# Kernel optimization log

Hardware: AMD Instinct MI355X
Metric: run time of the kernel (lower is better)

The kernel has to match this reference:

```python
import jax, jax.numpy as jnp
import numpy as np

N, E = 50000, 800000
ND, ED, HD = 128, 32, 256  # node_dim, edge_dim, hidden_dim

def silu(v):
    return v * jax.nn.sigmoid(v)

def setup_inputs() -> dict:
    key = jax.random.key(0)
    ks = jax.random.split(key, 16)
    s = lambda fan_in: 1.0 / np.sqrt(fan_in)
    inp = {
        'h': jax.random.normal(ks[0], (N, ND), jnp.float32),
        'x': jax.random.normal(ks[1], (N, 3), jnp.float32),
        'edge_index': jax.random.randint(ks[2], (2, E), 0, N, jnp.int64),
        'edge_attr': jax.random.normal(ks[3], (E, ED), jnp.float32),
        # msg_mlp: Linear(2*ND+1+ED, HD) -> SiLU -> Linear(HD, HD) -> SiLU
        'mW1': jax.random.normal(ks[4], (2 * ND + 1 + ED, HD), jnp.float32) * s(2 * ND + 1 + ED),
        'mb1': jnp.zeros((HD,), jnp.float32),
        'mW2': jax.random.normal(ks[5], (HD, HD), jnp.float32) * s(HD),
        'mb2': jnp.zeros((HD,), jnp.float32),
        # node_mlp: Linear(ND+HD, HD) -> SiLU -> Linear(HD, ND)
        'nW1': jax.random.normal(ks[6], (ND + HD, HD), jnp.float32) * s(ND + HD),
        'nb1': jnp.zeros((HD,), jnp.float32),
        'nW2': jax.random.normal(ks[7], (HD, ND), jnp.float32) * s(HD),
        'nb2': jnp.zeros((ND,), jnp.float32),
        # coord_mlp: Linear(HD, HD) -> SiLU -> Linear(HD, 1, bias=False)
        'cW1': jax.random.normal(ks[8], (HD, HD), jnp.float32) * s(HD),
        'cb1': jnp.zeros((HD,), jnp.float32),
        'cW2': jax.random.normal(ks[9], (HD, 1), jnp.float32) * s(HD),
        # LayerNorm(ND)
        'gamma': jnp.ones((ND,), jnp.float32),
        'beta': jnp.zeros((ND,), jnp.float32),
    }
    return inp

def reference(h, x, edge_index, edge_attr,
              mW1, mb1, mW2, mb2,
              nW1, nb1, nW2, nb2,
              cW1, cb1, cW2, gamma, beta):
    row, col = edge_index[0], edge_index[1]
    n = h.shape[0]
    dx = x[row] - x[col]                                   # [E,3]
    dist_sq = jnp.sum(dx * dx, axis=-1, keepdims=True) + 1e-8
    edge_in = jnp.concatenate([h[row], h[col], dist_sq, edge_attr], axis=-1)
    m = silu(edge_in @ mW1 + mb1)
    m = silu(m @ mW2 + mb2)                                # m_ij: [E,HD]
    m_i = jax.ops.segment_sum(m, row, num_segments=n)      # [N,HD]
    coef = silu(m @ cW1 + cb1) @ cW2                       # [E,1]
    x_agg = jax.ops.segment_sum(dx * coef, row, num_segments=n)
    x_out = x + x_agg
    h_in = jnp.concatenate([h, m_i], axis=-1)
    h_res = h + (silu(h_in @ nW1 + nb1) @ nW2 + nb2)
    mu = jnp.mean(h_res, axis=-1, keepdims=True)
    var = jnp.mean((h_res - mu) ** 2, axis=-1, keepdims=True)
    h_out = (h_res - mu) / jnp.sqrt(var + 1e-5) * gamma + beta
    return h_out, x_out
```

## Files before the change

kernel.cpp:

```cpp
#include <hip/hip_runtime.h>

#define ND 128
#define ED 32
#define HD 256
#define ASTR 296
#define NSTR 392

typedef short bf16x8 __attribute__((ext_vector_type(8)));
typedef float f32x4 __attribute__((ext_vector_type(4)));

__device__ __forceinline__ float silu_f(float v) {
  return v / (1.0f + __expf(-v));
}

__device__ __forceinline__ unsigned short bf_hi(float f) {
  unsigned int u = __float_as_uint(f);
  return (unsigned short)((u + 0x7FFFu + ((u >> 16) & 1u)) >> 16);
}
__device__ __forceinline__ float bf_to_f(unsigned short s) {
  return __uint_as_float(((unsigned int)s) << 16);
}
__device__ __forceinline__ void split2(float f, unsigned short& hi, unsigned short& lo) {
  hi = bf_hi(f);
  lo = bf_hi(f - bf_to_f(hi));
}
__device__ __forceinline__ void store_split4(unsigned short* hp, unsigned short* lp, float4 v) {
  ushort4 h4, l4;
  split2(v.x, h4.x, l4.x); split2(v.y, h4.y, l4.y);
  split2(v.z, h4.z, l4.z); split2(v.w, h4.w, l4.w);
  *reinterpret_cast<ushort4*>(hp) = h4;
  *reinterpret_cast<ushort4*>(lp) = l4;
}

__global__ void prep_frag(const float* __restrict__ W, unsigned short* __restrict__ Fh,
                          unsigned short* __restrict__ Fl, int Keff, int Ncols, int S,
                          int skiprow)
{
  int idx = blockIdx.x * 256 + threadIdx.x;
  int NT = Ncols >> 4;
  int total = S * NT * 64;
  if (idx >= total) return;
  int lane = idx & 63;
  int k0 = (idx / (NT * 64)) * 32 + ((lane >> 4) << 3);
  int n = ((idx >> 6) % NT) * 16 + (lane & 15);
  size_t base = (size_t)idx * 8;
  for (int j = 0; j < 8; ++j) {
    int k = k0 + j;
    float v = 0.f;
    if (k < Keff) {
      int wk = (skiprow >= 0 && k >= skiprow) ? (k + 1) : k;
      v = W[(size_t)wk * Ncols + n];
    }
    unsigned short hi, lo; split2(v, hi, lo);
    Fh[base + j] = hi; Fl[base + j] = lo;
  }
}

template<int STRIDE, int NT, int NTW>
__device__ __forceinline__ void mfma_gemm(const unsigned short* __restrict__ Ahi,
                                          const unsigned short* __restrict__ Alo,
                                          const unsigned short* __restrict__ Bh,
                                          const unsigned short* __restrict__ Bl,
                                          int S, int wave, int lane, f32x4 acc[4][NTW])
{
  const int tx = lane & 15, tz = lane >> 4;
  for (int s = 0; s < S; ++s) {
    bf16x8 bh[NTW], bl[NTW], ah[4], al[4];
    #pragma unroll
    for (int nt = 0; nt < NTW; ++nt) {
      size_t bidx = ((size_t)(s * NT + wave * NTW + nt) * 64 + lane) * 8;
      bh[nt] = *reinterpret_cast<const bf16x8*>(Bh + bidx);
      bl[nt] = *reinterpret_cast<const bf16x8*>(Bl + bidx);
    }
    const int koff = s * 32 + tz * 8;
    #pragma unroll
    for (int mt = 0; mt < 4; ++mt) {
      size_t aoff = (size_t)(mt * 16 + tx) * STRIDE + koff;
      ah[mt] = *reinterpret_cast<const bf16x8*>(Ahi + aoff);
      al[mt] = *reinterpret_cast<const bf16x8*>(Alo + aoff);
    }
    #pragma unroll
    for (int mt = 0; mt < 4; ++mt) {
      #pragma unroll
      for (int nt = 0; nt < NTW; ++nt) {
        acc[mt][nt] = __builtin_amdgcn_mfma_f32_16x16x32_bf16(ah[mt], bh[nt], acc[mt][nt], 0, 0, 0);
        acc[mt][nt] = __builtin_amdgcn_mfma_f32_16x16x32_bf16(ah[mt], bl[nt], acc[mt][nt], 0, 0, 0);
        acc[mt][nt] = __builtin_amdgcn_mfma_f32_16x16x32_bf16(al[mt], bh[nt], acc[mt][nt], 0, 0, 0);
      }
    }
  }
}

__global__ __launch_bounds__(512, 4)
void egnn_edge_mfma(const float* __restrict__ h, const float* __restrict__ x,
                    const int* __restrict__ eidx, const float* __restrict__ eattr,
                    const float* __restrict__ mW1, const float* __restrict__ mb1,
                    const float* __restrict__ mb2, const float* __restrict__ cb1,
                    const float* __restrict__ cW2,
                    const unsigned short* __restrict__ W1h, const unsigned short* __restrict__ W1l,
                    const unsigned short* __restrict__ W2h, const unsigned short* __restrict__ W2l,
                    const unsigned short* __restrict__ C1h, const unsigned short* __restrict__ C1l,
                    float* __restrict__ m_i, float* __restrict__ x_agg, int E)
{
  __shared__ unsigned short Ahi[64][ASTR];
  __shared__ unsigned short Alo[64][ASTR];
  __shared__ int   sRow[64];
  __shared__ float sDx0[64], sDx1[64], sDx2[64], sDist[64], sCoef[64];

  const int t  = threadIdx.x;
  const int e0 = blockIdx.x * 64;
  if (t < 64) sCoef[t] = 0.f;

  {
    const int e = t >> 3, part = t & 7;
    const int ge = e0 + e;
    if (ge < E) {
      const int r = eidx[ge], c = eidx[E + ge];
      const float* hsrc = (part < 4) ? (h + (size_t)r * ND + (part & 3) * 32)
                                     : (h + (size_t)c * ND + (part & 3) * 32);
      const int cb = (part < 4 ? 0 : 128) + (part & 3) * 32;
      #pragma unroll
      for (int i = 0; i < 8; ++i) {
        float4 v = reinterpret_cast<const float4*>(hsrc)[i];
        store_split4(&Ahi[e][cb + i * 4], &Alo[e][cb + i * 4], v);
      }
      float4 av = reinterpret_cast<const float4*>(eattr + (size_t)ge * ED)[part];
      store_split4(&Ahi[e][256 + part * 4], &Alo[e][256 + part * 4], av);
      if (part == 0) {
        sRow[e] = r;
        float d0 = x[3*(size_t)r+0] - x[3*(size_t)c+0];
        float d1 = x[3*(size_t)r+1] - x[3*(size_t)c+1];
        float d2 = x[3*(size_t)r+2] - x[3*(size_t)c+2];
        sDx0[e] = d0; sDx1[e] = d1; sDx2[e] = d2;
        sDist[e] = d0*d0 + d1*d1 + d2*d2 + 1e-8f;
      }
    }
  }
  __syncthreads();

  const int lane = t & 63, wave = t >> 6;
  const int tx = lane & 15, tz = lane >> 4;
  const int c0 = wave * 32 + tx;
  const int c1 = c0 + 16;

  f32x4 acc[4][2];

  {
    const float b0v = mb1[c0], b1v = mb1[c1];
    const float wA = mW1[(size_t)256 * HD + c0];
    const float wB = mW1[(size_t)256 * HD + c1];
    #pragma unroll
    for (int mt = 0; mt < 4; ++mt)
      #pragma unroll
      for (int r = 0; r < 4; ++r) {
        const float d = sDist[mt * 16 + tz * 4 + r];
        acc[mt][0][r] = b0v + d * wA;
        acc[mt][1][r] = b1v + d * wB;
      }
  }
  mfma_gemm<ASTR, 16, 2>(&Ahi[0][0], &Alo[0][0], W1h, W1l, 9, wave, lane, acc);
  __syncthreads();
  #pragma unroll
  for (int mt = 0; mt < 4; ++mt)
    #pragma unroll
    for (int r = 0; r < 4; ++r) {
      const int row = mt * 16 + tz * 4 + r;
      unsigned short hi, lo;
      split2(silu_f(acc[mt][0][r]), hi, lo);
      Ahi[row][c0] = hi; Alo[row][c0] = lo;
      split2(silu_f(acc[mt][1][r]), hi, lo);
      Ahi[row][c1] = hi; Alo[row][c1] = lo;
    }
  __syncthreads();

  {
    const float b0v = mb2[c0], b1v = mb2[c1];
    #pragma unroll
    for (int mt = 0; mt < 4; ++mt)
      #pragma unroll
      for (int r = 0; r < 4; ++r) { acc[mt][0][r] = b0v; acc[mt][1][r] = b1v; }
  }
  mfma_gemm<ASTR, 16, 2>(&Ahi[0][0], &Alo[0][0], W2h, W2l, 8, wave, lane, acc);
  #pragma unroll
  for (int mt = 0; mt < 4; ++mt)
    #pragma unroll
    for (int r = 0; r < 4; ++r) {
      acc[mt][0][r] = silu_f(acc[mt][0][r]);
      acc[mt][1][r] = silu_f(acc[mt][1][r]);
      const int row = mt * 16 + tz * 4 + r;
      if (e0 + row < E) {
        const size_t rn = (size_t)sRow[row] * HD;
        unsafeAtomicAdd(&m_i[rn + c0], acc[mt][0][r]);
        unsafeAtomicAdd(&m_i[rn + c1], acc[mt][1][r]);
      }
    }
  __syncthreads();
  #pragma unroll
  for (int mt = 0; mt < 4; ++mt)
    #pragma unroll
    for (int r = 0; r < 4; ++r) {
      const int row = mt * 16 + tz * 4 + r;
      unsigned short hi, lo;
      split2(acc[mt][0][r], hi, lo);
      Ahi[row][c0] = hi; Alo[row][c0] = lo;
      split2(acc[mt][1][r], hi, lo);
      Ahi[row][c1] = hi; Alo[row][c1] = lo;
    }
  __syncthreads();

  {
    const float b0v = cb1[c0], b1v = cb1[c1];
    #pragma unroll
    for (int mt = 0; mt < 4; ++mt)
      #pragma unroll
      for (int r = 0; r < 4; ++r) { acc[mt][0][r] = b0v; acc[mt][1][r] = b1v; }
  }
  mfma_gemm<ASTR, 16, 2>(&Ahi[0][0], &Alo[0][0], C1h, C1l, 8, wave, lane, acc);
  {
    const float w20 = cW2[c0], w21 = cW2[c1];
    #pragma unroll
    for (int mt = 0; mt < 4; ++mt)
      #pragma unroll
      for (int r = 0; r < 4; ++r) {
        float v = silu_f(acc[mt][0][r]) * w20 + silu_f(acc[mt][1][r]) * w21;
        v += __shfl_xor(v, 1); v += __shfl_xor(v, 2);
        v += __shfl_xor(v, 4); v += __shfl_xor(v, 8);
        if (tx == 0) atomicAdd(&sCoef[mt * 16 + tz * 4 + r], v);
      }
  }
  __syncthreads();
  if (t < 64 && e0 + t < E) {
    const float cf = sCoef[t];
    const size_t rn = 3 * (size_t)sRow[t];
    unsafeAtomicAdd(&x_agg[rn + 0], sDx0[t] * cf);
    unsafeAtomicAdd(&x_agg[rn + 1], sDx1[t] * cf);
    unsafeAtomicAdd(&x_agg[rn + 2], sDx2[t] * cf);
  }
}

__global__ __launch_bounds__(512, 2)
void egnn_node_mfma(const float* __restrict__ h, const float* __restrict__ m_i,
                    const unsigned short* __restrict__ N1h, const unsigned short* __restrict__ N1l,
                    const unsigned short* __restrict__ N2h, const unsigned short* __restrict__ N2l,
                    const float* __restrict__ nb1, const float* __restrict__ nb2,
                    const float* __restrict__ gamma, const float* __restrict__ beta,
                    float* __restrict__ hout, int N)
{
  __shared__ unsigned short Ahi[64][NSTR];
  __shared__ unsigned short Alo[64][NSTR];
  __shared__ float sSum[64], sSum2[64];

  const int t  = threadIdx.x;
  const int n0 = blockIdx.x * 64;
  if (t < 64) { sSum[t] = 0.f; sSum2[t] = 0.f; }

  {
    const int e = t >> 3, part = t & 7;
    const int n = n0 + e;
    if (n < N) {
      #pragma unroll
      for (int i = 0; i < 4; ++i) {
        float4 v = reinterpret_cast<const float4*>(h + (size_t)n * ND + part * 16)[i];
        store_split4(&Ahi[e][part * 16 + i * 4], &Alo[e][part * 16 + i * 4], v);
      }
      #pragma unroll
      for (int i = 0; i < 8; ++i) {
        float4 v = reinterpret_cast<const float4*>(m_i + (size_t)n * HD + part * 32)[i];
        store_split4(&Ahi[e][128 + part * 32 + i * 4], &Alo[e][128 + part * 32 + i * 4], v);
      }
    }
  }
  __syncthreads();

  const int lane = t & 63, wave = t >> 6;
  const int tx = lane & 15, tz = lane >> 4;

  {
    const int c0 = wave * 32 + tx, c1 = c0 + 16;
    f32x4 acc[4][2];
    const float b0v = nb1[c0], b1v = nb1[c1];
    #pragma unroll
    for (int mt = 0; mt < 4; ++mt)
      #pragma unroll
      for (int r = 0; r < 4; ++r) { acc[mt][0][r] = b0v; acc[mt][1][r] = b1v; }
    mfma_gemm<NSTR, 16, 2>(&Ahi[0][0], &Alo[0][0], N1h, N1l, 12, wave, lane, acc);
    __syncthreads();
    #pragma unroll
    for (int mt = 0; mt < 4; ++mt)
      #pragma unroll
      for (int r = 0; r < 4; ++r) {
        const int row = mt * 16 + tz * 4 + r;
        unsigned short hi, lo;
        split2(silu_f(acc[mt][0][r]), hi, lo);
        Ahi[row][c0] = hi; Alo[row][c0] = lo;
        split2(silu_f(acc[mt][1][r]), hi, lo);
        Ahi[row][c1] = hi; Alo[row][c1] = lo;
      }
    __syncthreads();
  }

  const int col = wave * 16 + tx;
  f32x4 a2[4][1];
  {
    const float bv = nb2[col];
    #pragma unroll
    for (int mt = 0; mt < 4; ++mt)
      #pragma unroll
      for (int r = 0; r < 4; ++r) a2[mt][0][r] = bv;
  }
  mfma_gemm<NSTR, 8, 1>(&Ahi[0][0], &Alo[0][0], N2h, N2l, 8, wave, lane, a2);

  const float g  = gamma[col];
  const float bt = beta[col];
  float vv[4][4];
  #pragma unroll
  for (int mt = 0; mt < 4; ++mt)
    #pragma unroll
    for (int r = 0; r < 4; ++r) {
      const int row = mt * 16 + tz * 4 + r;
      const int n = n0 + row;
      const float hv = (n < N) ? h[(size_t)n * ND + col] : 0.f;
      const float v = a2[mt][0][r] + hv;
      vv[mt][r] = v;
      float s1 = v, s2 = v * v;
      s1 += __shfl_xor(s1, 1); s1 += __shfl_xor(s1, 2);
      s1 += __shfl_xor(s1, 4); s1 += __shfl_xor(s1, 8);
      s2 += __shfl_xor(s2, 1); s2 += __shfl_xor(s2, 2);
      s2 += __shfl_xor(s2, 4); s2 += __shfl_xor(s2, 8);
      if (tx == 0) {
        atomicAdd(&sSum[row],  s1);
        atomicAdd(&sSum2[row], s2);
      }
    }
  __syncthreads();
  #pragma unroll
  for (int mt = 0; mt < 4; ++mt)
    #pragma unroll
    for (int r = 0; r < 4; ++r) {
      const int row = mt * 16 + tz * 4 + r;
      const int n = n0 + row;
      if (n < N) {
        const float mu   = sSum[row] * (1.f / 128.f);
        const float var  = sSum2[row] * (1.f / 128.f) - mu * mu;
        const float rstd = rsqrtf(var + 1e-5f);
        hout[(size_t)n * ND + col] = (vv[mt][r] - mu) * rstd * g + bt;
      }
    }
}

__global__ void egnn_xout_kernel(const float* __restrict__ x, const float* __restrict__ x_agg,
                                 float* __restrict__ xout, int total)
{
  int i = blockIdx.x * 256 + threadIdx.x;
  if (i < total) xout[i] = x[i] + x_agg[i];
}

extern "C" void kernel_launch(void* const* d_in, const int* in_sizes, int n_in,
                              void* d_out, int out_size, void* d_ws, size_t ws_size,
                              hipStream_t stream)
{
  const float* h     = (const float*)d_in[0];
  const float* x     = (const float*)d_in[1];
  const int*   eidx  = (const int*)  d_in[2];
  const float* eattr = (const float*)d_in[3];
  const float* mW1   = (const float*)d_in[4];
  const float* mb1   = (const float*)d_in[5];
  const float* mW2   = (const float*)d_in[6];
  const float* mb2   = (const float*)d_in[7];
  const float* nW1   = (const float*)d_in[8];
  const float* nb1   = (const float*)d_in[9];
  const float* nW2   = (const float*)d_in[10];
  const float* nb2   = (const float*)d_in[11];
  const float* cW1   = (const float*)d_in[12];
  const float* cb1   = (const float*)d_in[13];
  const float* cW2   = (const float*)d_in[14];
  const float* gamma = (const float*)d_in[15];
  const float* beta  = (const float*)d_in[16];

  const int N = in_sizes[0] / ND;
  const int E = in_sizes[2] / 2;

  float* m_i   = (float*)d_ws;
  float* x_agg = m_i + (size_t)N * HD;
  unsigned short* fr = (unsigned short*)(x_agg + (size_t)N * 3);

  const int SZ_W1 = 9  * 16 * 64 * 8;
  const int SZ_W2 = 8  * 16 * 64 * 8;
  const int SZ_N1 = 12 * 16 * 64 * 8;
  const int SZ_N2 = 8  * 8  * 64 * 8;
  unsigned short* W1h = fr; fr += SZ_W1;
  unsigned short* W1l = fr; fr += SZ_W1;
  unsigned short* W2h = fr; fr += SZ_W2;
  unsigned short* W2l = fr; fr += SZ_W2;
  unsigned short* C1h = fr; fr += SZ_W2;
  unsigned short* C1l = fr; fr += SZ_W2;
  unsigned short* N1h = fr; fr += SZ_N1;
  unsigned short* N1l = fr; fr += SZ_N1;
  unsigned short* N2h = fr; fr += SZ_N2;
  unsigned short* N2l = fr; fr += SZ_N2;

  float* hout = (float*)d_out;
  float* xout = hout + (size_t)N * ND;

  hipMemsetAsync(m_i,   0, (size_t)N * HD * sizeof(float), stream);
  hipMemsetAsync(x_agg, 0, (size_t)N * 3  * sizeof(float), stream);

  prep_frag<<<(9*16*64  + 255)/256, 256, 0, stream>>>(mW1, W1h, W1l, 288, 256,  9, 256);
  prep_frag<<<(8*16*64  + 255)/256, 256, 0, stream>>>(mW2, W2h, W2l, 256, 256,  8,  -1);
  prep_frag<<<(8*16*64  + 255)/256, 256, 0, stream>>>(cW1, C1h, C1l, 256, 256,  8,  -1);
  prep_frag<<<(12*16*64 + 255)/256, 256, 0, stream>>>(nW1, N1h, N1l, 384, 256, 12,  -1);
  prep_frag<<<(8*8*64   + 255)/256, 256, 0, stream>>>(nW2, N2h, N2l, 256, 128,  8,  -1);

  egnn_edge_mfma<<<(E + 63) / 64, 512, 0, stream>>>(
      h, x, eidx, eattr, mW1, mb1, mb2, cb1, cW2,
      W1h, W1l, W2h, W2l, C1h, C1l, m_i, x_agg, E);
  egnn_node_mfma<<<(N + 63) / 64, 512, 0, stream>>>(
      h, m_i, N1h, N1l, N2h, N2l, nb1, nb2, gamma, beta, hout, N);
  egnn_xout_kernel<<<(N * 3 + 255) / 256, 256, 0, stream>>>(x, x_agg, xout, N * 3);
}
```

Baseline: 1.415 ms.

## Presplit node features to bf16 hi/lo, use hardware bf16 convert, unroll GEMM

Adds a presplit kernel that converts h into bf16 hi/lo arrays once, so the edge and node kernels copy pre-split halves instead of re-splitting the gathered features per edge. Replaces the software round-to-nearest bf16 split with the v_cvt_pk_bf16_f32 instruction. Makes the GEMM k-step count a template parameter with full unrolling and raises wave priority around the MFMA block with s_setprio. It also moves the m_i atomics after the LDS write of the second-layer output. The trade-offs are an extra kernel and workspace buffer, more registers and code from the unroll, and possible rounding-mode differences in the conversion.

```diff
diff --git a/kernel.cpp b/kernel.cpp
--- a/kernel.cpp
+++ b/kernel.cpp
@@ -13,23 +13,38 @@
   return v / (1.0f + __expf(-v));
 }
 
-__device__ __forceinline__ unsigned short bf_hi(float f) {
-  unsigned int u = __float_as_uint(f);
-  return (unsigned short)((u + 0x7FFFu + ((u >> 16) & 1u)) >> 16);
-}
-__device__ __forceinline__ float bf_to_f(unsigned short s) {
-  return __uint_as_float(((unsigned int)s) << 16);
-}
-__device__ __forceinline__ void split2(float f, unsigned short& hi, unsigned short& lo) {
-  hi = bf_hi(f);
-  lo = bf_hi(f - bf_to_f(hi));
+__device__ __forceinline__ unsigned int cvt_pk_bf16(float a, float b) {
+  unsigned int r;
+  asm("v_cvt_pk_bf16_f32 %0, %1, %2" : "=v"(r) : "v"(a), "v"(b));
+  return r;
+}
+__device__ __forceinline__ void split_pk(float f0, float f1, unsigned int& hw, unsigned int& lw) {
+  hw = cvt_pk_bf16(f0, f1);
+  float h0 = __uint_as_float(hw << 16);
+  float h1 = __uint_as_float(hw & 0xFFFF0000u);
+  lw = cvt_pk_bf16(f0 - h0, f1 - h1);
+}
+__device__ __forceinline__ void split1(float v, unsigned short& hs, unsigned short& ls) {
+  unsigned int hw = cvt_pk_bf16(v, v);
+  float hf = __uint_as_float(hw << 16);
+  unsigned int lw = cvt_pk_bf16(v - hf, v - hf);
+  hs = (unsigned short)hw; ls = (unsigned short)lw;
 }
 __device__ __forceinline__ void store_split4(unsigned short* hp, unsigned short* lp, float4 v) {
-  ushort4 h4, l4;
-  split2(v.x, h4.x, l4.x); split2(v.y, h4.y, l4.y);
-  split2(v.z, h4.z, l4.z); split2(v.w, h4.w, l4.w);
-  *reinterpret_cast<ushort4*>(hp) = h4;
-  *reinterpret_cast<ushort4*>(lp) = l4;
+  unsigned int hw0, lw0, hw1, lw1;
+  split_pk(v.x, v.y, hw0, lw0);
+  split_pk(v.z, v.w, hw1, lw1);
+  *reinterpret_cast<uint2*>(hp) = make_uint2(hw0, hw1);
+  *reinterpret_cast<uint2*>(lp) = make_uint2(lw0, lw1);
+}
+
+__global__ void presplit_kernel(const float* __restrict__ src, unsigned short* __restrict__ dh,
+                                unsigned short* __restrict__ dl, int total4)
+{
+  int i = blockIdx.x * 256 + threadIdx.x;
+  if (i >= total4) return;
+  float4 v = reinterpret_cast<const float4*>(src)[i];
+  store_split4(dh + (size_t)i * 4, dl + (size_t)i * 4, v);
 }
 
 __global__ void prep_frag(const float* __restrict__ W, unsigned short* __restrict__ Fh,
@@ -51,19 +66,20 @@
       int wk = (skiprow >= 0 && k >= skiprow) ? (k + 1) : k;
       v = W[(size_t)wk * Ncols + n];
     }
-    unsigned short hi, lo; split2(v, hi, lo);
+    unsigned short hi, lo; split1(v, hi, lo);
     Fh[base + j] = hi; Fl[base + j] = lo;
   }
 }
 
-template<int STRIDE, int NT, int NTW>
-__device__ __forceinline__ void mfma_gemm(const unsigned short* __restrict__ Ahi,
-                                          const unsigned short* __restrict__ Alo,
+template<int STRIDE, int NT, int NTW, int S>
+__device__ __forceinline__ void mfma_gemm(const unsigned short* __restrict__ Ahi_,
+                                          const unsigned short* __restrict__ Alo_,
                                           const unsigned short* __restrict__ Bh,
                                           const unsigned short* __restrict__ Bl,
-                                          int S, int wave, int lane, f32x4 acc[4][NTW])
+                                          int wave, int lane, f32x4 acc[4][NTW])
 {
   const int tx = lane & 15, tz = lane >> 4;
+  #pragma unroll
   for (int s = 0; s < S; ++s) {
     bf16x8 bh[NTW], bl[NTW], ah[4], al[4];
     #pragma unroll
@@ -76,9 +92,10 @@
     #pragma unroll
     for (int mt = 0; mt < 4; ++mt) {
       size_t aoff = (size_t)(mt * 16 + tx) * STRIDE + koff;
-      ah[mt] = *reinterpret_cast<const bf16x8*>(Ahi + aoff);
-      al[mt] = *reinterpret_cast<const bf16x8*>(Alo + aoff);
-    }
+      ah[mt] = *reinterpret_cast<const bf16x8*>(Ahi_ + aoff);
+      al[mt] = *reinterpret_cast<const bf16x8*>(Alo_ + aoff);
+    }
+    __builtin_amdgcn_s_setprio(1);
     #pragma unroll
     for (int mt = 0; mt < 4; ++mt) {
       #pragma unroll
@@ -88,11 +105,13 @@
         acc[mt][nt] = __builtin_amdgcn_mfma_f32_16x16x32_bf16(al[mt], bh[nt], acc[mt][nt], 0, 0, 0);
       }
     }
+    __builtin_amdgcn_s_setprio(0);
   }
 }
 
 __global__ __launch_bounds__(512, 4)
-void egnn_edge_mfma(const float* __restrict__ h, const float* __restrict__ x,
+void egnn_edge_mfma(const unsigned short* __restrict__ Hh, const unsigned short* __restrict__ Hl,
+                    const float* __restrict__ x,
                     const int* __restrict__ eidx, const float* __restrict__ eattr,
                     const float* __restrict__ mW1, const float* __restrict__ mb1,
                     const float* __restrict__ mb2, const float* __restrict__ cb1,
@@ -116,13 +135,13 @@
     const int ge = e0 + e;
     if (ge < E) {
       const int r = eidx[ge], c = eidx[E + ge];
-      const float* hsrc = (part < 4) ? (h + (size_t)r * ND + (part & 3) * 32)
-                                     : (h + (size_t)c * ND + (part & 3) * 32);
+      const int node = (part < 4) ? r : c;
       const int cb = (part < 4 ? 0 : 128) + (part & 3) * 32;
-      #pragma unroll
-      for (int i = 0; i < 8; ++i) {
-        float4 v = reinterpret_cast<const float4*>(hsrc)[i];
-        store_split4(&Ahi[e][cb + i * 4], &Alo[e][cb + i * 4], v);
+      const size_t gb = (size_t)node * ND + (part & 3) * 32;
+      #pragma unroll
+      for (int i = 0; i < 4; ++i) {
+        reinterpret_cast<uint4*>(&Ahi[e][cb])[i] = reinterpret_cast<const uint4*>(Hh + gb)[i];
+        reinterpret_cast<uint4*>(&Alo[e][cb])[i] = reinterpret_cast<const uint4*>(Hl + gb)[i];
       }
       float4 av = reinterpret_cast<const float4*>(eattr + (size_t)ge * ED)[part];
       store_split4(&Ahi[e][256 + part * 4], &Alo[e][256 + part * 4], av);
@@ -158,18 +177,18 @@
         acc[mt][1][r] = b1v + d * wB;
       }
   }
-  mfma_gemm<ASTR, 16, 2>(&Ahi[0][0], &Alo[0][0], W1h, W1l, 9, wave, lane, acc);
+  mfma_gemm<ASTR, 16, 2, 9>(&Ahi[0][0], &Alo[0][0], W1h, W1l, wave, lane, acc);
   __syncthreads();
   #pragma unroll
   for (int mt = 0; mt < 4; ++mt)
     #pragma unroll
     for (int r = 0; r < 4; ++r) {
       const int row = mt * 16 + tz * 4 + r;
-      unsigned short hi, lo;
-      split2(silu_f(acc[mt][0][r]), hi, lo);
-      Ahi[row][c0] = hi; Alo[row][c0] = lo;
-      split2(silu_f(acc[mt][1][r]), hi, lo);
-      Ahi[row][c1] = hi; Alo[row][c1] = lo;
+      unsigned short hs, ls;
+      split1(silu_f(acc[mt][0][r]), hs, ls);
+      Ahi[row][c0] = hs; Alo[row][c0] = ls;
+      split1(silu_f(acc[mt][1][r]), hs, ls);
+      Ahi[row][c1] = hs; Alo[row][c1] = ls;
     }
   __syncthreads();
 
@@ -180,13 +199,32 @@
       #pragma unroll
       for (int r = 0; r < 4; ++r) { acc[mt][0][r] = b0v; acc[mt][1][r] = b1v; }
   }
-  mfma_gemm<ASTR, 16, 2>(&Ahi[0][0], &Alo[0][0], W2h, W2l, 8, wave, lane, acc);
+  mfma_gemm<ASTR, 16, 2, 8>(&Ahi[0][0], &Alo[0][0], W2h, W2l, wave, lane, acc);
   #pragma unroll
   for (int mt = 0; mt < 4; ++mt)
     #pragma unroll
     for (int r = 0; r < 4; ++r) {
       acc[mt][0][r] = silu_f(acc[mt][0][r]);
       acc[mt][1][r] = silu_f(acc[mt][1][r]);
+    }
+  __syncthreads();
+  #pragma unroll
+  for (int mt = 0; mt < 4; ++mt)
+    #pragma unroll
+    for (int r = 0; r < 4; ++r) {
+      const int row = mt * 16 + tz * 4 + r;
+      unsigned short hs, ls;
+      split1(acc[mt][0][r], hs, ls);
+      Ahi[row][c0] = hs; Alo[row][c0] = ls;
+      split1(acc[mt][1][r], hs, ls);
+      Ahi[row][c1] = hs; Alo[row][c1] = ls;
+    }
+  __syncthreads();
+
+  #pragma unroll
+  for (int mt = 0; mt < 4; ++mt)
+    #pragma unroll
+    for (int r = 0; r < 4; ++r) {
       const int row = mt * 16 + tz * 4 + r;
       if (e0 + row < E) {
         const size_t rn = (size_t)sRow[row] * HD;
@@ -194,19 +232,6 @@
         unsafeAtomicAdd(&m_i[rn + c1], acc[mt][1][r]);
       }
     }
-  __syncthreads();
-  #pragma unroll
-  for (int mt = 0; mt < 4; ++mt)
-    #pragma unroll
-    for (int r = 0; r < 4; ++r) {
-      const int row = mt * 16 + tz * 4 + r;
-      unsigned short hi, lo;
-      split2(acc[mt][0][r], hi, lo);
-      Ahi[row][c0] = hi; Alo[row][c0] = lo;
-      split2(acc[mt][1][r], hi, lo);
-      Ahi[row][c1] = hi; Alo[row][c1] = lo;
-    }
-  __syncthreads();
 
   {
     const float b0v = cb1[c0], b1v = cb1[c1];
@@ -215,7 +240,7 @@
       #pragma unroll
       for (int r = 0; r < 4; ++r) { acc[mt][0][r] = b0v; acc[mt][1][r] = b1v; }
   }
-  mfma_gemm<ASTR, 16, 2>(&Ahi[0][0], &Alo[0][0], C1h, C1l, 8, wave, lane, acc);
+  mfma_gemm<ASTR, 16, 2, 8>(&Ahi[0][0], &Alo[0][0], C1h, C1l, wave, lane, acc);
   {
     const float w20 = cW2[c0], w21 = cW2[c1];
     #pragma unroll
@@ -239,7 +264,9 @@
 }
 
 __global__ __launch_bounds__(512, 2)
-void egnn_node_mfma(const float* __restrict__ h, const float* __restrict__ m_i,
+void egnn_node_mfma(const float* __restrict__ h,
+                    const unsigned short* __restrict__ Hh, const unsigned short* __restrict__ Hl,
+                    const float* __restrict__ m_i,
                     const unsigned short* __restrict__ N1h, const unsigned short* __restrict__ N1l,
                     const unsigned short* __restrict__ N2h, const unsigned short* __restrict__ N2l,
                     const float* __restrict__ nb1, const float* __restrict__ nb2,
@@ -258,10 +285,11 @@
     const int e = t >> 3, part = t & 7;
     const int n = n0 + e;
     if (n < N) {
-      #pragma unroll
-      for (int i = 0; i < 4; ++i) {
-        float4 v = reinterpret_cast<const float4*>(h + (size_t)n * ND + part * 16)[i];
-        store_split4(&Ahi[e][part * 16 + i * 4], &Alo[e][part * 16 + i * 4], v);
+      const size_t gb = (size_t)n * ND + part * 16;
+      #pragma unroll
+      for (int i = 0; i < 2; ++i) {
+        reinterpret_cast<uint4*>(&Ahi[e][part * 16])[i] = reinterpret_cast<const uint4*>(Hh + gb)[i];
+        reinterpret_cast<uint4*>(&Alo[e][part * 16])[i] = reinterpret_cast<const uint4*>(Hl + gb)[i];
       }
       #pragma unroll
       for (int i = 0; i < 8; ++i) {
@@ -283,18 +311,18 @@
     for (int mt = 0; mt < 4; ++mt)
       #pragma unroll
       for (int r = 0; r < 4; ++r) { acc[mt][0][r] = b0v; acc[mt][1][r] = b1v; }
-    mfma_gemm<NSTR, 16, 2>(&Ahi[0][0], &Alo[0][0], N1h, N1l, 12, wave, lane, acc);
+    mfma_gemm<NSTR, 16, 2, 12>(&Ahi[0][0], &Alo[0][0], N1h, N1l, wave, lane, acc);
     __syncthreads();
     #pragma unroll
     for (int mt = 0; mt < 4; ++mt)
       #pragma unroll
       for (int r = 0; r < 4; ++r) {
         const int row = mt * 16 + tz * 4 + r;
-        unsigned short hi, lo;
-        split2(silu_f(acc[mt][0][r]), hi, lo);
-        Ahi[row][c0] = hi; Alo[row][c0] = lo;
-        split2(silu_f(acc[mt][1][r]), hi, lo);
-        Ahi[row][c1] = hi; Alo[row][c1] = lo;
+        unsigned short hs, ls;
+        split1(silu_f(acc[mt][0][r]), hs, ls);
+        Ahi[row][c0] = hs; Alo[row][c0] = ls;
+        split1(silu_f(acc[mt][1][r]), hs, ls);
+        Ahi[row][c1] = hs; Alo[row][c1] = ls;
       }
     __syncthreads();
   }
@@ -308,7 +336,7 @@
       #pragma unroll
       for (int r = 0; r < 4; ++r) a2[mt][0][r] = bv;
   }
-  mfma_gemm<NSTR, 8, 1>(&Ahi[0][0], &Alo[0][0], N2h, N2l, 8, wave, lane, a2);
+  mfma_gemm<NSTR, 8, 1, 8>(&Ahi[0][0], &Alo[0][0], N2h, N2l, wave, lane, a2);
 
   const float g  = gamma[col];
   const float bt = beta[col];
@@ -384,6 +412,9 @@
   float* x_agg = m_i + (size_t)N * HD;
   unsigned short* fr = (unsigned short*)(x_agg + (size_t)N * 3);
 
+  unsigned short* Hh = fr; fr += (size_t)N * ND;
+  unsigned short* Hl = fr; fr += (size_t)N * ND;
+
   const int SZ_W1 = 9  * 16 * 64 * 8;
   const int SZ_W2 = 8  * 16 * 64 * 8;
   const int SZ_N1 = 12 * 16 * 64 * 8;
@@ -405,6 +436,7 @@
   hipMemsetAsync(m_i,   0, (size_t)N * HD * sizeof(float), stream);
   hipMemsetAsync(x_agg, 0, (size_t)N * 3  * sizeof(float), stream);
 
+  presplit_kernel<<<(N * ND / 4 + 255)/256, 256, 0, stream>>>(h, Hh, Hl, N * ND / 4);
   prep_frag<<<(9*16*64  + 255)/256, 256, 0, stream>>>(mW1, W1h, W1l, 288, 256,  9, 256);
   prep_frag<<<(8*16*64  + 255)/256, 256, 0, stream>>>(mW2, W2h, W2l, 256, 256,  8,  -1);
   prep_frag<<<(8*16*64  + 255)/256, 256, 0, stream>>>(cW1, C1h, C1l, 256, 256,  8,  -1);
@@ -412,9 +444,9 @@
   prep_frag<<<(8*8*64   + 255)/256, 256, 0, stream>>>(nW2, N2h, N2l, 256, 128,  8,  -1);
 
   egnn_edge_mfma<<<(E + 63) / 64, 512, 0, stream>>>(
-      h, x, eidx, eattr, mW1, mb1, mb2, cb1, cW2,
+      Hh, Hl, x, eidx, eattr, mW1, mb1, mb2, cb1, cW2,
       W1h, W1l, W2h, W2l, C1h, C1l, m_i, x_agg, E);
   egnn_node_mfma<<<(N + 63) / 64, 512, 0, stream>>>(
-      h, m_i, N1h, N1l, N2h, N2l, nb1, nb2, gamma, beta, hout, N);
+      h, Hh, Hl, m_i, N1h, N1l, N2h, N2l, nb1, nb2, gamma, beta, hout, N);
   egnn_xout_kernel<<<(N * 3 + 255) / 256, 256, 0, stream>>>(x, x_agg, xout, N * 3);
 }
```

Result: slower. 1.573 ms (+11.1%).
